# Kernel optimization log

Hardware: AMD Instinct MI355X
Metric: run time of the kernel (lower is better)

The kernel has to match this reference:

```python
import jax, jax.numpy as jnp
import numpy as np

DIM = 1536
HEADS = 12
HEAD_DIM = DIM // HEADS
EPS = 1e-6
IMG_LEN = 257


def _rmsnorm(x, g):
    var = jnp.mean(jnp.square(x), axis=-1, keepdims=True)
    return x * jax.lax.rsqrt(var + EPS) * g


def _attn(q, k, v):
    # q: [b, Lq, h, d], k/v: [b, Lk, h, d]
    scale = 1.0 / jnp.sqrt(jnp.asarray(HEAD_DIM, q.dtype))
    s = jnp.einsum('bqhd,bkhd->bhqk', q, k) * scale
    p = jax.nn.softmax(s, axis=-1)
    return jnp.einsum('bhqk,bkhd->bqhd', p, v)


def setup_inputs() -> dict:
    key = jax.random.key(0)
    ks = jax.random.split(key, 20)
    w = lambda k: jax.random.normal(k, (DIM, DIM), dtype=jnp.float32) * 0.02
    b = lambda k: jax.random.normal(k, (DIM,), dtype=jnp.float32) * 0.01
    return {
        'x': jax.random.normal(ks[0], (1, 16384, DIM), dtype=jnp.float32),
        'context': jax.random.normal(ks[1], (1, 769, DIM), dtype=jnp.float32),
        'context_lens': jax.random.randint(ks[2], (1,), 0, 512, dtype=jnp.int32),
        'Wq': w(ks[3]), 'bq': b(ks[4]),
        'Wk': w(ks[5]), 'bk': b(ks[6]),
        'Wv': w(ks[7]), 'bv': b(ks[8]),
        'W_addk': w(ks[9]), 'b_addk': b(ks[10]),
        'W_addv': w(ks[11]), 'b_addv': b(ks[12]),
        'Wo': w(ks[13]), 'bo': b(ks[14]),
        'gq': jnp.ones((DIM,), dtype=jnp.float32),
        'gk': jnp.ones((DIM,), dtype=jnp.float32),
        'g_addk': jnp.ones((DIM,), dtype=jnp.float32),
    }


def reference(x, context, context_lens, Wq, bq, Wk, bk, Wv, bv,
              W_addk, b_addk, W_addv, b_addv, Wo, bo, gq, gk, g_addk):
    b_sz, L1, _ = x.shape
    ctx_img = context[:, :IMG_LEN]   # [B, 257, C]
    ctx_txt = context[:, IMG_LEN:]   # [B, L2-257, C]

    q = _rmsnorm(x @ Wq + bq, gq).reshape(b_sz, -1, HEADS, HEAD_DIM)
    k = _rmsnorm(ctx_txt @ Wk + bk, gk).reshape(b_sz, -1, HEADS, HEAD_DIM)
    v = (ctx_txt @ Wv + bv).reshape(b_sz, -1, HEADS, HEAD_DIM)
    k_img = _rmsnorm(ctx_img @ W_addk + b_addk, g_addk).reshape(b_sz, -1, HEADS, HEAD_DIM)
    v_img = (ctx_img @ W_addv + b_addv).reshape(b_sz, -1, HEADS, HEAD_DIM)

    img_x = _attn(q, k_img, v_img).reshape(b_sz, L1, DIM)
    txt_x = _attn(q, k, v).reshape(b_sz, L1, DIM)
    out = (txt_x + img_x) @ Wo + bo
    return out
```

## Files before the change

### kernel.cpp

```cpp
#include <hip/hip_runtime.h>
#include <cstdint>
#include <cstddef>

typedef unsigned short u16;
typedef unsigned int u32;
typedef short bfrag __attribute__((ext_vector_type(8)));
typedef __bf16 yfrag __attribute__((ext_vector_type(8)));
typedef float f4 __attribute__((ext_vector_type(4)));

__device__ __forceinline__ u16 f2bs(float f) {
  union { float f; u32 u; } x; x.f = f;
  u32 r = x.u + 0x7fffu + ((x.u >> 16) & 1u);
  return (u16)(r >> 16);
}
__device__ __forceinline__ float bs2f(u16 s) {
  union { u32 u; float f; } x; x.u = ((u32)s) << 16;
  return x.f;
}
__device__ __forceinline__ u32 cvtpk_bf16(float lo, float hi) {
  u32 d;
  asm("v_cvt_pk_bf16_f32 %0, %1, %2" : "=v"(d) : "v"(lo), "v"(hi));
  return d;
}

template <typename T>
__device__ __forceinline__ auto mfma_sel(T a, T b, f4 c, int)
    -> decltype(__builtin_amdgcn_mfma_f32_16x16x32_bf16(a, b, c, 0, 0, 0)) {
  return __builtin_amdgcn_mfma_f32_16x16x32_bf16(a, b, c, 0, 0, 0);
}
template <typename T>
__device__ __forceinline__ f4 mfma_sel(T a, T b, f4 c, long) {
  yfrag ya = __builtin_bit_cast(yfrag, a);
  yfrag yb = __builtin_bit_cast(yfrag, b);
  return __builtin_amdgcn_mfma_f32_16x16x32_bf16(ya, yb, c, 0, 0, 0);
}
__device__ __forceinline__ f4 MFMA(bfrag a, bfrag b, f4 c) {
  return mfma_sel(a, b, c, 0);
}

__device__ __forceinline__ void gl2lds16(const u16* g, u16* l) {
  __builtin_amdgcn_global_load_lds(
      (__attribute__((address_space(1))) void*)(g),
      (__attribute__((address_space(3))) void*)(l), 16, 0, 0);
}

__global__ __launch_bounds__(256) void cvt2(const float* __restrict__ x,
                                            u16* __restrict__ xbf,
                                            const float* __restrict__ ctx,
                                            u16* __restrict__ ctxb) {
  int i = blockIdx.x * 256 + threadIdx.x;
  const float* src; u16* dst;
  if (i < 3145728) {
    src = x; dst = xbf;
  } else {
    i -= 3145728;
    if (i >= 147648) return;
    src = ctx; dst = ctxb;
  }
  const float4* s4 = (const float4*)src;
  float4 a = s4[(size_t)i * 2];
  float4 b = s4[(size_t)i * 2 + 1];
  uint4 o;
  o.x = cvtpk_bf16(a.x, a.y);
  o.y = cvtpk_bf16(a.z, a.w);
  o.z = cvtpk_bf16(b.x, b.y);
  o.w = cvtpk_bf16(b.z, b.w);
  ((uint4*)dst)[i] = o;
}

__global__ __launch_bounds__(256) void transpose6(
    const float* s0, const float* s1, const float* s2, const float* s3,
    const float* s4, const float* s5, u16* d0, u16* d1, u16* d2, u16* d3,
    u16* d4, u16* d5) {
  const float* src; u16* dst;
  switch (blockIdx.z) {
    case 0: src = s0; dst = d0; break;
    case 1: src = s1; dst = d1; break;
    case 2: src = s2; dst = d2; break;
    case 3: src = s3; dst = d3; break;
    case 4: src = s4; dst = d4; break;
    default: src = s5; dst = d5; break;
  }
  __shared__ float tile[32][33];
  int tx = threadIdx.x, ty = threadIdx.y;
  int bx = blockIdx.x * 32, by = blockIdx.y * 32;
#pragma unroll
  for (int j = 0; j < 4; j++)
    tile[ty + j * 8][tx] = src[(size_t)(by + ty + j * 8) * 1536 + bx + tx];
  __syncthreads();
#pragma unroll
  for (int j = 0; j < 4; j++)
    dst[(size_t)(bx + ty + j * 8) * 1536 + by + tx] = f2bs(tile[tx][ty + j * 8]);
}

__device__ __forceinline__ void gemm256_core(
    const u16* __restrict__ A, const u16* __restrict__ Bt,
    const float* __restrict__ bias, void* __restrict__ outp,
    int Mreal, int ldT, int epi, int bx, int by, u16* As, u16* Bs) {
  const int tid = threadIdx.x;
  const int w = tid >> 6, lane = tid & 63;
  const int quad = lane >> 4, l15 = lane & 15;
  const int wm = w >> 2, wn = w & 3;
  const int m0 = bx * 256, n0 = by * 256;

  f4 acc[8][4];
#pragma unroll
  for (int i = 0; i < 8; i++)
#pragma unroll
    for (int j = 0; j < 4; j++) acc[i][j] = f4{0.f, 0.f, 0.f, 0.f};

  const int r0 = tid >> 2;
  const int c0s = ((tid & 3) ^ (r0 & 3)) * 8;
  const int r1 = r0 + 128;
  const int c1s = ((tid & 3) ^ (r1 & 3)) * 8;
  const u16* Ab = A + (size_t)m0 * 1536;
  const u16* Bb = Bt + (size_t)n0 * 1536;

#define STAGE_A(t)                                                        \
  {                                                                       \
    const int s_ = (t) & 3, k_ = (t) * 32;                                \
    gl2lds16(Ab + (size_t)r0 * 1536 + k_ + c0s, As + s_ * 8192 + w * 512);\
    gl2lds16(Ab + (size_t)r1 * 1536 + k_ + c1s,                           \
             As + s_ * 8192 + 4096 + w * 512);                            \
  }
#define STAGE_B(t)                                                        \
  {                                                                       \
    const int s_ = (t) & 3, k_ = (t) * 32;                                \
    gl2lds16(Bb + (size_t)r0 * 1536 + k_ + c0s, Bs + s_ * 8192 + w * 512);\
    gl2lds16(Bb + (size_t)r1 * 1536 + k_ + c1s,                           \
             Bs + s_ * 8192 + 4096 + w * 512);                            \
  }

  STAGE_A(0); STAGE_B(0);
  STAGE_A(1); STAGE_B(1);
  STAGE_A(2); STAGE_B(2);

  for (int kt = 0; kt < 48; ++kt) {
    const int s = kt & 3;
    const u16* Asb = As + s * 8192;
    const u16* Bsb = Bs + s * 8192;
    if (kt < 46)
      asm volatile("s_waitcnt vmcnt(8)" ::: "memory");
    else if (kt == 46)
      asm volatile("s_waitcnt vmcnt(4)" ::: "memory");
    else
      asm volatile("s_waitcnt vmcnt(0)" ::: "memory");
    asm volatile("s_waitcnt lgkmcnt(0)" ::: "memory");
    asm volatile("s_barrier" ::: "memory");

    bfrag af[8], bf[4];
#pragma unroll
    for (int nf = 0; nf < 4; nf++) {
      const int rb = wn * 64 + nf * 16 + l15;
      bf[nf] = *(const bfrag*)(Bsb + rb * 32 + ((quad ^ (rb & 3)) * 8));
    }
#pragma unroll
    for (int mf = 0; mf < 4; mf++) {
      const int r = wm * 128 + mf * 16 + l15;
      af[mf] = *(const bfrag*)(Asb + r * 32 + ((quad ^ (r & 3)) * 8));
    }
    if (kt < 45) STAGE_A(kt + 3);
    __builtin_amdgcn_s_setprio(1);
#pragma unroll
    for (int mf = 0; mf < 4; mf++)
#pragma unroll
      for (int nf = 0; nf < 4; nf++)
        acc[mf][nf] = MFMA(af[mf], bf[nf], acc[mf][nf]);
    __builtin_amdgcn_s_setprio(0);

    asm volatile("s_waitcnt lgkmcnt(0)" ::: "memory");
    asm volatile("s_barrier" ::: "memory");
#pragma unroll
    for (int mf = 4; mf < 8; mf++) {
      const int r = wm * 128 + mf * 16 + l15;
      af[mf] = *(const bfrag*)(Asb + r * 32 + ((quad ^ (r & 3)) * 8));
    }
    if (kt < 45) STAGE_B(kt + 3);
    __builtin_amdgcn_s_setprio(1);
#pragma unroll
    for (int mf = 4; mf < 8; mf++)
#pragma unroll
      for (int nf = 0; nf < 4; nf++)
        acc[mf][nf] = MFMA(af[mf], bf[nf], acc[mf][nf]);
    __builtin_amdgcn_s_setprio(0);
  }
#undef STAGE_A
#undef STAGE_B

  float bcol[4];
#pragma unroll
  for (int nf = 0; nf < 4; nf++) bcol[nf] = bias[n0 + wn * 64 + nf * 16 + l15];

  if (epi == 1) {
    u16* dst = (u16*)outp;
#pragma unroll
    for (int mf = 0; mf < 8; mf++)
#pragma unroll
      for (int r = 0; r < 4; r++) {
        int row = m0 + wm * 128 + mf * 16 + quad * 4 + r;
        if (row < Mreal) {
#pragma unroll
          for (int nf = 0; nf < 4; nf++) {
            int col = n0 + wn * 64 + nf * 16 + l15;
            dst[(size_t)col * ldT + row] = f2bs(acc[mf][nf][r] + bcol[nf]);
          }
        }
      }
  } else if (epi == 0) {
    u16* dst = (u16*)outp;
#pragma unroll
    for (int mf = 0; mf < 8; mf++)
#pragma unroll
      for (int r = 0; r < 4; r++) {
        int row = m0 + wm * 128 + mf * 16 + quad * 4 + r;
        if (row < Mreal) {
#pragma unroll
          for (int nf = 0; nf < 4; nf++) {
            int col = n0 + wn * 64 + nf * 16 + l15;
            dst[(size_t)row * 1536 + col] = f2bs(acc[mf][nf][r] + bcol[nf]);
          }
        }
      }
  } else {
    float* dst = (float*)outp;
#pragma unroll
    for (int mf = 0; mf < 8; mf++)
#pragma unroll
      for (int r = 0; r < 4; r++) {
        int row = m0 + wm * 128 + mf * 16 + quad * 4 + r;
        if (row < Mreal) {
#pragma unroll
          for (int nf = 0; nf < 4; nf++) {
            int col = n0 + wn * 64 + nf * 16 + l15;
            dst[(size_t)row * 1536 + col] = acc[mf][nf][r] + bcol[nf];
          }
        }
      }
  }
}

__global__ __launch_bounds__(512, 2) void gemm256(
    const u16* __restrict__ xbf, const u16* __restrict__ wqT,
    const float* __restrict__ bq, u16* __restrict__ qb,
    const u16* __restrict__ ctxb, const u16* __restrict__ wkT,
    const float* __restrict__ bk, u16* __restrict__ ktxt,
    const u16* __restrict__ wakT, const float* __restrict__ bak,
    u16* __restrict__ kimg, const u16* __restrict__ wvT,
    const float* __restrict__ bv, u16* __restrict__ vtt,
    const u16* __restrict__ wavT, const float* __restrict__ bav,
    u16* __restrict__ vti, const u16* __restrict__ yb,
    const u16* __restrict__ woT, const float* __restrict__ bo,
    float* __restrict__ out, int mode) {
  extern __shared__ u16 lds[];
  u16* As = lds;
  u16* Bs = lds + 32768;
  const int id = blockIdx.x;
  const u16* ctxt = ctxb + 257 * 1536;
  const u16* A; const u16* Bt; const float* bias; void* outp;
  int Mreal, ldT, epi, bx, by;
  if (mode == 1) {
    A = yb; Bt = woT; bias = bo; outp = out;
    Mreal = 16384; ldT = 0; epi = 2; bx = id & 63; by = id >> 6;
  } else if (id < 384) {
    A = xbf; Bt = wqT; bias = bq; outp = qb;
    Mreal = 16384; ldT = 0; epi = 0; bx = id & 63; by = id >> 6;
  } else if (id < 396) {
    int t = id - 384;
    A = ctxt; Bt = wkT; bias = bk; outp = ktxt;
    Mreal = 512; ldT = 0; epi = 0; bx = t & 1; by = t >> 1;
  } else if (id < 408) {
    int t = id - 396;
    A = ctxb; Bt = wakT; bias = bak; outp = kimg;
    Mreal = 257; ldT = 0; epi = 0; bx = t & 1; by = t >> 1;
  } else if (id < 420) {
    int t = id - 408;
    A = ctxt; Bt = wvT; bias = bv; outp = vtt;
    Mreal = 512; ldT = 512; epi = 1; bx = t & 1; by = t >> 1;
  } else {
    int t = id - 420;
    A = ctxb; Bt = wavT; bias = bav; outp = vti;
    Mreal = 257; ldT = 264; epi = 1; bx = t & 1; by = t >> 1;
  }
  gemm256_core(A, Bt, bias, outp, Mreal, ldT, epi, bx, by, As, Bs);
}

__global__ __launch_bounds__(256) void rmsnorm_multi(
    u16* __restrict__ qb, const float* __restrict__ gq,
    u16* __restrict__ ktxt, const float* __restrict__ gk,
    u16* __restrict__ kimg, const float* __restrict__ gak) {
  int row = blockIdx.x;
  u16* buf; const float* g;
  if (row < 16384) {
    buf = qb; g = gq;
  } else if (row < 16896) {
    buf = ktxt; g = gk; row -= 16384;
  } else {
    buf = kimg; g = gak; row -= 16896;
  }
  const int tid = threadIdx.x;
  u32* p = (u32*)(buf + (size_t)row * 1536);
  const float2* g2 = (const float2*)g;
  u32 d[3];
  float v[6];
  float ss = 0.f;
#pragma unroll
  for (int j = 0; j < 3; j++) {
    d[j] = p[tid + j * 256];
    v[2 * j]     = bs2f((u16)(d[j] & 0xffffu));
    v[2 * j + 1] = bs2f((u16)(d[j] >> 16));
    ss += v[2 * j] * v[2 * j] + v[2 * j + 1] * v[2 * j + 1];
  }
#pragma unroll
  for (int off = 32; off; off >>= 1) ss += __shfl_xor(ss, off);
  __shared__ float red[4];
  if ((tid & 63) == 0) red[tid >> 6] = ss;
  __syncthreads();
  ss = red[0] + red[1] + red[2] + red[3];
  const float sc = rsqrtf(ss * (1.0f / 1536.0f) + 1e-6f);
#pragma unroll
  for (int j = 0; j < 3; j++) {
    float2 gg = g2[tid + j * 256];
    p[tid + j * 256] =
        cvtpk_bf16(v[2 * j] * sc * gg.x, v[2 * j + 1] * sc * gg.y);
  }
}

#define ATTN_SCALE 0.08838834764831845f
__global__ __launch_bounds__(256, 2) void attn_kernel(
    const u16* __restrict__ q, const u16* __restrict__ ktxt,
    const u16* __restrict__ kimg, const u16* __restrict__ vttxt,
    const u16* __restrict__ vtimg, u16* __restrict__ y) {
  __shared__ u16 Ks[64 * 128];
  __shared__ u16 Vs[128 * 64];
  __shared__ u16 Ps[4 * 32 * 72];
  const int tid = threadIdx.x;
  const int w = tid >> 6, lane = tid & 63;
  const int quad = lane >> 4, l15 = lane & 15;
  const int h = blockIdx.y, hoff = h * 128;
  const int mw = blockIdx.x * 128 + w * 32;
  u16* Pw = Ps + w * (32 * 72);

  bfrag qf[2][4];
#pragma unroll
  for (int rt = 0; rt < 2; rt++) {
    const u16* qrow = q + (size_t)(mw + rt * 16 + l15) * 1536 + hoff + quad * 8;
#pragma unroll
    for (int c = 0; c < 4; c++) qf[rt][c] = *(const bfrag*)(qrow + c * 32);
  }

  int kko[4], kco[4], vfe[4], vco[4];
#pragma unroll
  for (int j = 0; j < 4; j++) {
    int i = j * 256 + tid;
    int s = i >> 4, cp = i & 15;
    kko[j] = 4 * (s & 15) + (s >> 4);
    kco[j] = ((cp ^ (s & 7)) * 8);
    int f = i >> 3, cq = i & 7;
    vfe[j] = f;
    vco[j] = ((cq ^ (f & 7)) * 8);
  }

  f4 o[2][8];
  u32 resA[2][8][2];
  float lr[2][4];

  for (int seg = 0; seg < 2; seg++) {
    const u16* kp = seg ? ktxt : kimg;
    const u16* vp = seg ? vttxt : vtimg;
    const int Lk = seg ? 512 : 257;
    const int ldv = seg ? 512 : 264;
    const int nit = seg ? 8 : 5;
#pragma unroll
    for (int rt = 0; rt < 2; rt++) {
#pragma unroll
      for (int ft = 0; ft < 8; ft++) o[rt][ft] = f4{0.f, 0.f, 0.f, 0.f};
#pragma unroll
      for (int r = 0; r < 4; r++) lr[rt][r] = 0.f;
    }

    for (int it = 0; it < nit; ++it) {
      const int t0 = it * 64;
#pragma unroll
      for (int j = 0; j < 4; j++)
        gl2lds16(kp + (size_t)(t0 + kko[j]) * 1536 + hoff + kco[j],
                 Ks + (j * 256 + w * 64) * 8);
#pragma unroll
      for (int j = 0; j < 4; j++)
        gl2lds16(vp + (size_t)(hoff + vfe[j]) * ldv + t0 + vco[j],
                 Vs + (j * 256 + w * 64) * 8);
      __syncthreads();

      f4 s[2][4];
#pragma unroll
      for (int rt = 0; rt < 2; rt++)
#pragma unroll
        for (int t = 0; t < 4; t++) s[rt][t] = f4{0.f, 0.f, 0.f, 0.f};
#pragma unroll
      for (int t = 0; t < 4; t++) {
        const u16* kb = Ks + (t * 16 + l15) * 128;
        bfrag kf[4];
#pragma unroll
        for (int c = 0; c < 4; c++)
          kf[c] = *(const bfrag*)(kb + (((c * 4 + quad) ^ (l15 & 7)) * 8));
#pragma unroll
        for (int rt = 0; rt < 2; rt++)
#pragma unroll
          for (int c = 0; c < 4; c++)
            s[rt][t] = MFMA(qf[rt][c], kf[c], s[rt][t]);
      }

      if (t0 + 64 <= Lk) {
#pragma unroll
        for (int rt = 0; rt < 2; rt++)
#pragma unroll
          for (int t = 0; t < 4; t++)
#pragma unroll
            for (int r = 0; r < 4; r++) {
              float p = __expf(s[rt][t][r] * ATTN_SCALE);
              s[rt][t][r] = p;
              lr[rt][r] += p;
            }
      } else {
#pragma unroll
        for (int t = 0; t < 4; t++) {
          bool ok = (t0 + 4 * l15 + t) < Lk;
#pragma unroll
          for (int rt = 0; rt < 2; rt++)
#pragma unroll
            for (int r = 0; r < 4; r++) {
              float p = ok ? __expf(s[rt][t][r] * ATTN_SCALE) : 0.f;
              s[rt][t][r] = p;
              lr[rt][r] += p;
            }
        }
      }

#pragma unroll
      for (int rt = 0; rt < 2; rt++)
#pragma unroll
        for (int r = 0; r < 4; r++) {
          u32 lo = cvtpk_bf16(s[rt][0][r], s[rt][1][r]);
          u32 hi = cvtpk_bf16(s[rt][2][r], s[rt][3][r]);
          *(uint2*)(Pw + (rt * 16 + quad * 4 + r) * 72 + l15 * 4) =
              make_uint2(lo, hi);
        }
      asm volatile("s_waitcnt lgkmcnt(0)" ::: "memory");
      bfrag pf[2][2];
#pragma unroll
      for (int rt = 0; rt < 2; rt++)
#pragma unroll
        for (int hf = 0; hf < 2; hf++)
          pf[rt][hf] =
              *(const bfrag*)(Pw + (rt * 16 + l15) * 72 + hf * 32 + quad * 8);

#pragma unroll
      for (int ft = 0; ft < 8; ft++) {
        const u16* vb = Vs + (ft * 16 + l15) * 64;
#pragma unroll
        for (int hf = 0; hf < 2; hf++) {
          bfrag vf = *(const bfrag*)(vb + (((hf * 4 + quad) ^ (l15 & 7)) * 8));
#pragma unroll
          for (int rt = 0; rt < 2; rt++)
            o[rt][ft] = MFMA(pf[rt][hf], vf, o[rt][ft]);
        }
      }
      __syncthreads();
    }

#pragma unroll
    for (int rt = 0; rt < 2; rt++)
#pragma unroll
      for (int r = 0; r < 4; r++) {
        float v = lr[rt][r];
        v += __shfl_xor(v, 1);
        v += __shfl_xor(v, 2);
        v += __shfl_xor(v, 4);
        v += __shfl_xor(v, 8);
        lr[rt][r] = 1.0f / v;
      }
    if (seg == 0) {
#pragma unroll
      for (int rt = 0; rt < 2; rt++)
#pragma unroll
        for (int ft = 0; ft < 8; ft++) {
          resA[rt][ft][0] = cvtpk_bf16(o[rt][ft][0] * lr[rt][0],
                                       o[rt][ft][1] * lr[rt][1]);
          resA[rt][ft][1] = cvtpk_bf16(o[rt][ft][2] * lr[rt][2],
                                       o[rt][ft][3] * lr[rt][3]);
        }
    }
  }

#pragma unroll
  for (int rt = 0; rt < 2; rt++)
#pragma unroll
    for (int ft = 0; ft < 8; ft++) {
      float ra[4];
      ra[0] = bs2f((u16)(resA[rt][ft][0] & 0xffffu));
      ra[1] = bs2f((u16)(resA[rt][ft][0] >> 16));
      ra[2] = bs2f((u16)(resA[rt][ft][1] & 0xffffu));
      ra[3] = bs2f((u16)(resA[rt][ft][1] >> 16));
#pragma unroll
      for (int r = 0; r < 4; r++)
        y[(size_t)(mw + rt * 16 + quad * 4 + r) * 1536 + hoff + ft * 16 + l15] =
            f2bs(ra[r] + o[rt][ft][r] * lr[rt][r]);
    }
}

extern "C" void kernel_launch(void* const* d_in, const int* in_sizes, int n_in,
                              void* d_out, int out_size, void* d_ws,
                              size_t ws_size, hipStream_t stream) {
  const float* x   = (const float*)d_in[0];
  const float* ctx = (const float*)d_in[1];
  const float* Wq  = (const float*)d_in[3];
  const float* bq  = (const float*)d_in[4];
  const float* Wk  = (const float*)d_in[5];
  const float* bk  = (const float*)d_in[6];
  const float* Wv  = (const float*)d_in[7];
  const float* bv  = (const float*)d_in[8];
  const float* Wak = (const float*)d_in[9];
  const float* bak = (const float*)d_in[10];
  const float* Wav = (const float*)d_in[11];
  const float* bav = (const float*)d_in[12];
  const float* Wo  = (const float*)d_in[13];
  const float* bo  = (const float*)d_in[14];
  const float* gq  = (const float*)d_in[15];
  const float* gk  = (const float*)d_in[16];
  const float* gak = (const float*)d_in[17];
  float* out = (float*)d_out;

  u16* xbf  = (u16*)d_ws;
  u16* qb   = xbf + 25165824;
  u16* ctxb = qb + 25165824;
  u16* wqT  = ctxb + 1181184;
  u16* wkT  = wqT + 2359296;
  u16* wvT  = wkT + 2359296;
  u16* wakT = wvT + 2359296;
  u16* wavT = wakT + 2359296;
  u16* woT  = wavT + 2359296;
  u16* ktxt = woT + 2359296;
  u16* kimg = ktxt + 786432;
  u16* vti  = kimg + 394752;
  u16* vtt  = vti + 405504;

  cvt2<<<12865, 256, 0, stream>>>(x, xbf, ctx, ctxb);
  transpose6<<<dim3(48, 48, 6), dim3(32, 8), 0, stream>>>(
      Wq, Wk, Wv, Wak, Wav, Wo, wqT, wkT, wvT, wakT, wavT, woT);

  gemm256<<<432, 512, 131072, stream>>>(xbf, wqT, bq, qb,
                                        ctxb, wkT, bk, ktxt,
                                        wakT, bak, kimg,
                                        wvT, bv, vtt,
                                        wavT, bav, vti,
                                        xbf, woT, bo, out, 0);

  rmsnorm_multi<<<17153, 256, 0, stream>>>(qb, gq, ktxt, gk, kimg, gak);

  attn_kernel<<<dim3(128, 12), 256, 0, stream>>>(qb, ktxt, kimg, vtt, vti, xbf);

  gemm256<<<384, 512, 131072, stream>>>(xbf, wqT, bq, qb,
                                        ctxb, wkT, bk, ktxt,
                                        wakT, bak, kimg,
                                        wvT, bv, vtt,
                                        wavT, bav, vti,
                                        xbf, woT, bo, out, 1);
}
```

Baseline: 575.5 us.

## Switch GEMM mainloop to double-buffered 64-wide K tiles and XCD-aware block remap

Restructures the 256x256 GEMM mainloop from a 4-stage pipeline of 32-wide K slices into a 2-stage pipeline of 64-wide K slices, with a wider XOR swizzle (8 chunks) and fewer barriers per K step. Global-to-LDS staging of the next tile is issued after both halves of fragments are read, and all 8 A fragments are loaded at once. Block IDs are also remapped so consecutive logical tiles land on the same XCD for better L2 sharing. This trades prefetch depth for fewer synchronisations, and the remap assumes the grid size is divisible by 8.

```diff
diff --git a/kernel.cpp b/kernel.cpp
--- a/kernel.cpp
+++ b/kernel.cpp
@@ -109,83 +109,73 @@
 #pragma unroll
     for (int j = 0; j < 4; j++) acc[i][j] = f4{0.f, 0.f, 0.f, 0.f};
 
-  const int r0 = tid >> 2;
-  const int c0s = ((tid & 3) ^ (r0 & 3)) * 8;
-  const int r1 = r0 + 128;
-  const int c1s = ((tid & 3) ^ (r1 & 3)) * 8;
+  const int rbase = w * 8 + (lane >> 3);
+  const int csrc = ((lane & 7) ^ (lane >> 3)) * 8;
   const u16* Ab = A + (size_t)m0 * 1536;
   const u16* Bb = Bt + (size_t)n0 * 1536;
 
-#define STAGE_A(t)                                                        \
-  {                                                                       \
-    const int s_ = (t) & 3, k_ = (t) * 32;                                \
-    gl2lds16(Ab + (size_t)r0 * 1536 + k_ + c0s, As + s_ * 8192 + w * 512);\
-    gl2lds16(Ab + (size_t)r1 * 1536 + k_ + c1s,                           \
-             As + s_ * 8192 + 4096 + w * 512);                            \
-  }
-#define STAGE_B(t)                                                        \
-  {                                                                       \
-    const int s_ = (t) & 3, k_ = (t) * 32;                                \
-    gl2lds16(Bb + (size_t)r0 * 1536 + k_ + c0s, Bs + s_ * 8192 + w * 512);\
-    gl2lds16(Bb + (size_t)r1 * 1536 + k_ + c1s,                           \
-             Bs + s_ * 8192 + 4096 + w * 512);                            \
-  }
-
-  STAGE_A(0); STAGE_B(0);
-  STAGE_A(1); STAGE_B(1);
-  STAGE_A(2); STAGE_B(2);
-
-  for (int kt = 0; kt < 48; ++kt) {
-    const int s = kt & 3;
-    const u16* Asb = As + s * 8192;
-    const u16* Bsb = Bs + s * 8192;
-    if (kt < 46)
-      asm volatile("s_waitcnt vmcnt(8)" ::: "memory");
-    else if (kt == 46)
-      asm volatile("s_waitcnt vmcnt(4)" ::: "memory");
+#define STG(Gb, Ls, t)                                                      \
+  {                                                                         \
+    u16* d_ = (Ls) + ((t) & 1) * 16384;                                     \
+    const u16* s_ = (Gb) + (size_t)(t) * 64 + csrc;                         \
+    _Pragma("unroll")                                                       \
+    for (int j = 0; j < 4; j++)                                             \
+      gl2lds16(s_ + (size_t)(j * 64 + rbase) * 1536,                        \
+               d_ + (j * 512 + w * 64) * 8);                                \
+  }
+
+  STG(Ab, As, 0); STG(Bb, Bs, 0);
+  STG(Ab, As, 1); STG(Bb, Bs, 1);
+
+  for (int kt = 0; kt < 24; ++kt) {
+    const u16* Asb = As + (kt & 1) * 16384;
+    const u16* Bsb = Bs + (kt & 1) * 16384;
+    if (kt < 23)
+      asm volatile("s_waitcnt vmcnt(8)\n\ts_barrier" ::: "memory");
     else
-      asm volatile("s_waitcnt vmcnt(0)" ::: "memory");
-    asm volatile("s_waitcnt lgkmcnt(0)" ::: "memory");
-    asm volatile("s_barrier" ::: "memory");
+      asm volatile("s_waitcnt vmcnt(0)\n\ts_barrier" ::: "memory");
 
     bfrag af[8], bf[4];
 #pragma unroll
     for (int nf = 0; nf < 4; nf++) {
-      const int rb = wn * 64 + nf * 16 + l15;
-      bf[nf] = *(const bfrag*)(Bsb + rb * 32 + ((quad ^ (rb & 3)) * 8));
-    }
-#pragma unroll
-    for (int mf = 0; mf < 4; mf++) {
-      const int r = wm * 128 + mf * 16 + l15;
-      af[mf] = *(const bfrag*)(Asb + r * 32 + ((quad ^ (r & 3)) * 8));
-    }
-    if (kt < 45) STAGE_A(kt + 3);
+      const int R = wn * 64 + nf * 16 + l15;
+      bf[nf] = *(const bfrag*)(Bsb + R * 64 + ((quad ^ (R & 7)) * 8));
+    }
+#pragma unroll
+    for (int mf = 0; mf < 8; mf++) {
+      const int R = wm * 128 + mf * 16 + l15;
+      af[mf] = *(const bfrag*)(Asb + R * 64 + ((quad ^ (R & 7)) * 8));
+    }
     __builtin_amdgcn_s_setprio(1);
 #pragma unroll
-    for (int mf = 0; mf < 4; mf++)
+    for (int mf = 0; mf < 8; mf++)
 #pragma unroll
       for (int nf = 0; nf < 4; nf++)
         acc[mf][nf] = MFMA(af[mf], bf[nf], acc[mf][nf]);
     __builtin_amdgcn_s_setprio(0);
 
-    asm volatile("s_waitcnt lgkmcnt(0)" ::: "memory");
-    asm volatile("s_barrier" ::: "memory");
-#pragma unroll
-    for (int mf = 4; mf < 8; mf++) {
-      const int r = wm * 128 + mf * 16 + l15;
-      af[mf] = *(const bfrag*)(Asb + r * 32 + ((quad ^ (r & 3)) * 8));
-    }
-    if (kt < 45) STAGE_B(kt + 3);
+    bfrag af1[8], bf1[4];
+#pragma unroll
+    for (int nf = 0; nf < 4; nf++) {
+      const int R = wn * 64 + nf * 16 + l15;
+      bf1[nf] = *(const bfrag*)(Bsb + R * 64 + (((4 + quad) ^ (R & 7)) * 8));
+    }
+#pragma unroll
+    for (int mf = 0; mf < 8; mf++) {
+      const int R = wm * 128 + mf * 16 + l15;
+      af1[mf] = *(const bfrag*)(Asb + R * 64 + (((4 + quad) ^ (R & 7)) * 8));
+    }
+    asm volatile("s_waitcnt lgkmcnt(0)\n\ts_barrier" ::: "memory");
+    if (kt < 22) { STG(Ab, As, kt + 2); STG(Bb, Bs, kt + 2); }
     __builtin_amdgcn_s_setprio(1);
 #pragma unroll
-    for (int mf = 4; mf < 8; mf++)
+    for (int mf = 0; mf < 8; mf++)
 #pragma unroll
       for (int nf = 0; nf < 4; nf++)
-        acc[mf][nf] = MFMA(af[mf], bf[nf], acc[mf][nf]);
+        acc[mf][nf] = MFMA(af1[mf], bf1[nf], acc[mf][nf]);
     __builtin_amdgcn_s_setprio(0);
   }
-#undef STAGE_A
-#undef STAGE_B
+#undef STG
 
   float bcol[4];
 #pragma unroll
@@ -254,7 +244,8 @@
   extern __shared__ u16 lds[];
   u16* As = lds;
   u16* Bs = lds + 32768;
-  const int id = blockIdx.x;
+  const int cpx = gridDim.x >> 3;
+  int id = (blockIdx.x & 7) * cpx + (blockIdx.x >> 3);
   const u16* ctxt = ctxb + 257 * 1536;
   const u16* A; const u16* Bt; const float* bias; void* outp;
   int Mreal, ldT, epi, bx, by;
```

New measurement: 575.9 us. Within noise of the previous version (+0.1%).
